# Optimization experiments

Measured on AMD Instinct MI355X. Metric: run time of the kernel, lower is better.

## Reference

```python
import jax, jax.numpy as jnp
import numpy as np

B, L, D, H, DK, DV = 512, 256, 1024, 16, 64, 64
TEMP = float(np.sqrt(D))  # source uses sqrt(d_model), not sqrt(d_k)
LN_EPS = 1.0              # LayerNormalization default eps=1, added to std


def setup_inputs() -> dict:
    key = jax.random.key(0)
    ks = jax.random.split(key, 7)
    u = lambda k, shape: jax.random.uniform(k, shape, jnp.float32, -0.04, 0.04)
    return {
        "q": jax.random.normal(ks[0], (B, D), jnp.float32),
        "k": jax.random.normal(ks[1], (B, L, D), jnp.float32),
        "v": jax.random.normal(ks[2], (B, L, D), jnp.float32),
        "Wq": u(ks[3], (H, DK, D)),   # stacked per-head q-proj weights
        "Wk": u(ks[4], (H, DK, D)),
        "Wv": u(ks[5], (H, DV, D)),
        "Wp": u(ks[6], (D, H * DV)),  # output projection (nn.Linear weight layout)
        "scale": jnp.ones((D,), jnp.float32),
        "offset": jnp.zeros((D,), jnp.float32),
    }


def reference(q, k, v, Wq, Wk, Wv, Wp, scale, offset):
    # per-head projections (batched over heads instead of a Python loop)
    hq = jnp.einsum('bd,hkd->bhk', q, Wq)       # [B,H,DK]
    hk = jnp.einsum('bld,hkd->bhlk', k, Wk)     # [B,H,L,DK]
    hv = jnp.einsum('bld,hvd->bhlv', v, Wv)     # [B,H,L,DV]
    # single-query dot-product attention per head
    scores = jnp.einsum('bhk,bhlk->bhl', hq, hk) / TEMP
    w = jax.nn.softmax(scores, axis=-1)         # dropout is identity (rate 0 / eval)
    ctx = jnp.einsum('bhl,bhlv->bhv', w, hv).reshape(B, H * DV)
    # output projection + residual
    out = ctx @ Wp.T + q
    # LayerNormalization: unbiased std (torch.std default), eps added to std
    mean = out.mean(axis=-1, keepdims=True)
    std = jnp.sqrt(jnp.sum((out - mean) ** 2, axis=-1, keepdims=True) / (D - 1))
    return scale * (out - mean) / (std + LN_EPS) + offset
```

## Files before the change

kernel.cpp:

```cpp
#include <hip/hip_runtime.h>

#define B_ 512
#define L_ 256
#define D_ 1024
#define H_ 16
#define DK_ 64
#define DV_ 64

typedef float f32x4 __attribute__((ext_vector_type(4)));
typedef __bf16 bf16x8 __attribute__((ext_vector_type(8)));

#define MFMA16(a, b, c) __builtin_amdgcn_mfma_f32_16x16x32_bf16((a), (b), (c), 0, 0, 0)

__device__ inline bf16x8 cvt8(f32x4 a, f32x4 b) {
  bf16x8 r;
  r[0] = (__bf16)a[0]; r[1] = (__bf16)a[1]; r[2] = (__bf16)a[2]; r[3] = (__bf16)a[3];
  r[4] = (__bf16)b[0]; r[5] = (__bf16)b[1]; r[6] = (__bf16)b[2]; r[7] = (__bf16)b[3];
  return r;
}

__global__ __launch_bounds__(256) void k_hq(const float* __restrict__ q,
                                            const float* __restrict__ Wq,
                                            __bf16* __restrict__ hq) {
  int tid = threadIdx.x, lane = tid & 63, wid = tid >> 6;
  int r16 = lane & 15, g = lane >> 4;
  int n0 = (blockIdx.x * 4 + wid) * 16;
  int m0 = blockIdx.y * 16;
  const float* arow = q  + (size_t)(m0 + r16) * D_;
  const float* brow = Wq + (size_t)(n0 + r16) * D_;
  f32x4 acc = {0.f, 0.f, 0.f, 0.f};
  for (int ks = 0; ks < D_ / 32; ++ks) {
    int k0 = ks * 32 + g * 8;
    f32x4 a0 = *(const f32x4*)(arow + k0);
    f32x4 a1 = *(const f32x4*)(arow + k0 + 4);
    f32x4 b0 = *(const f32x4*)(brow + k0);
    f32x4 b1 = *(const f32x4*)(brow + k0 + 4);
    acc = MFMA16(cvt8(a0, a1), cvt8(b0, b1), acc);
  }
#pragma unroll
  for (int r = 0; r < 4; ++r) {
    int m = m0 + g * 4 + r;
    hq[(size_t)m * (H_ * DK_) + n0 + r16] = (__bf16)acc[r];
  }
}

__global__ __launch_bounds__(256) void k_aq(const __bf16* __restrict__ hq,
                                            const float* __restrict__ Wk,
                                            __bf16* __restrict__ Aq) {
  int tid = threadIdx.x, lane = tid & 63, wid = tid >> 6;
  int r16 = lane & 15, g = lane >> 4;
  int h = blockIdx.z;
  int n0 = (blockIdx.x * 4 + wid) * 16;
  int m0 = blockIdx.y * 16;
  const __bf16* arow = hq + (size_t)(m0 + r16) * (H_ * DK_) + h * DK_;
  const float* bcol = Wk + (size_t)h * DK_ * D_ + n0 + r16;
  f32x4 acc = {0.f, 0.f, 0.f, 0.f};
#pragma unroll
  for (int ks = 0; ks < 2; ++ks) {
    int k0 = ks * 32 + g * 8;
    bf16x8 a = *(const bf16x8*)(arow + k0);
    f32x4 c0, c1;
#pragma unroll
    for (int j = 0; j < 4; ++j) c0[j] = bcol[(size_t)(k0 + j) * D_];
#pragma unroll
    for (int j = 0; j < 4; ++j) c1[j] = bcol[(size_t)(k0 + 4 + j) * D_];
    acc = MFMA16(a, cvt8(c0, c1), acc);
  }
#pragma unroll
  for (int r = 0; r < 4; ++r) {
    int m = m0 + g * 4 + r;
    Aq[(size_t)m * (H_ * D_) + (size_t)h * D_ + n0 + r16] = (__bf16)acc[r];
  }
}

__global__ __launch_bounds__(512) void k_attn(const float* __restrict__ kg,
                                              const float* __restrict__ vg,
                                              const __bf16* __restrict__ Aq,
                                              __bf16* __restrict__ cv) {
  __shared__ float  s_lds[H_][L_ + 4];
  __shared__ __bf16 w_lds[H_][L_ + 8];

  int b = blockIdx.x;
  int tid = threadIdx.x, lane = tid & 63, wv = tid >> 6;
  int r16 = lane & 15, g = lane >> 4;
  const __bf16* AqB = Aq + (size_t)b * H_ * D_;
  const float*  kB  = kg + (size_t)b * L_ * D_;
  const float*  vB  = vg + (size_t)b * L_ * D_;

  f32x4 accA[2] = {{0.f,0.f,0.f,0.f}, {0.f,0.f,0.f,0.f}};
  for (int ks = 0; ks < D_ / 32; ++ks) {
    int k0 = ks * 32 + g * 8;
    bf16x8 a = *(const bf16x8*)(AqB + (size_t)r16 * D_ + k0);
#pragma unroll
    for (int nt = 0; nt < 2; ++nt) {
      int l = wv * 32 + nt * 16 + r16;
      const float* p = kB + (size_t)l * D_ + k0;
      accA[nt] = MFMA16(a, cvt8(*(const f32x4*)p, *(const f32x4*)(p + 4)), accA[nt]);
    }
  }
  const float inv_temp = 1.0f / 32.0f;
#pragma unroll
  for (int nt = 0; nt < 2; ++nt)
#pragma unroll
    for (int r = 0; r < 4; ++r)
      s_lds[g * 4 + r][wv * 32 + nt * 16 + r16] = accA[nt][r] * inv_temp;
  __syncthreads();

#pragma unroll
  for (int rr = 0; rr < 2; ++rr) {
    int row = wv * 2 + rr;
    float x0 = s_lds[row][lane];
    float x1 = s_lds[row][lane + 64];
    float x2 = s_lds[row][lane + 128];
    float x3 = s_lds[row][lane + 192];
    float m = fmaxf(fmaxf(x0, x1), fmaxf(x2, x3));
#pragma unroll
    for (int off = 32; off; off >>= 1) m = fmaxf(m, __shfl_xor(m, off));
    float e0 = __expf(x0 - m), e1 = __expf(x1 - m);
    float e2 = __expf(x2 - m), e3 = __expf(x3 - m);
    float s = e0 + e1 + e2 + e3;
#pragma unroll
    for (int off = 32; off; off >>= 1) s += __shfl_xor(s, off);
    float inv = 1.0f / s;
    w_lds[row][lane]       = (__bf16)(e0 * inv);
    w_lds[row][lane + 64]  = (__bf16)(e1 * inv);
    w_lds[row][lane + 128] = (__bf16)(e2 * inv);
    w_lds[row][lane + 192] = (__bf16)(e3 * inv);
  }
  __syncthreads();

  bf16x8 afr[8];
#pragma unroll
  for (int ksl = 0; ksl < 8; ++ksl)
    afr[ksl] = *(const bf16x8*)(&w_lds[r16][ksl * 32 + g * 8]);

#pragma unroll
  for (int nt = 0; nt < 8; ++nt) {
    int d = wv * 128 + nt * 16 + r16;
    f32x4 c = {0.f, 0.f, 0.f, 0.f};
#pragma unroll
    for (int ksl = 0; ksl < 8; ++ksl) {
      int l0 = ksl * 32 + g * 8;
      const float* p = vB + (size_t)l0 * D_ + d;
      f32x4 c0, c1;
#pragma unroll
      for (int j = 0; j < 4; ++j) c0[j] = p[(size_t)j * D_];
#pragma unroll
      for (int j = 0; j < 4; ++j) c1[j] = p[(size_t)(4 + j) * D_];
      c = MFMA16(afr[ksl], cvt8(c0, c1), c);
    }
#pragma unroll
    for (int r = 0; r < 4; ++r)
      cv[(size_t)b * (H_ * D_) + (size_t)(g * 4 + r) * D_ + d] = (__bf16)c[r];
  }
}

__global__ __launch_bounds__(256) void k_ctx(const __bf16* __restrict__ cv,
                                             const float* __restrict__ Wv,
                                             __bf16* __restrict__ ctx) {
  int tid = threadIdx.x, lane = tid & 63, wid = tid >> 6;
  int r16 = lane & 15, g = lane >> 4;
  int h = blockIdx.z, m0 = blockIdx.y * 16, n0 = wid * 16;
  const __bf16* arow = cv + (size_t)(m0 + r16) * (H_ * D_) + (size_t)h * D_;
  const float* brow = Wv + (size_t)h * DV_ * D_ + (size_t)(n0 + r16) * D_;
  f32x4 acc = {0.f, 0.f, 0.f, 0.f};
  for (int ks = 0; ks < D_ / 32; ++ks) {
    int k0 = ks * 32 + g * 8;
    bf16x8 a = *(const bf16x8*)(arow + k0);
    f32x4 b0 = *(const f32x4*)(brow + k0);
    f32x4 b1 = *(const f32x4*)(brow + k0 + 4);
    acc = MFMA16(a, cvt8(b0, b1), acc);
  }
#pragma unroll
  for (int r = 0; r < 4; ++r) {
    int m = m0 + g * 4 + r;
    ctx[(size_t)m * (H_ * DV_) + h * DV_ + n0 + r16] = (__bf16)acc[r];
  }
}

__global__ __launch_bounds__(256) void k_out(const __bf16* __restrict__ ctx,
                                             const float* __restrict__ Wp,
                                             const float* __restrict__ q,
                                             float* __restrict__ outp) {
  int tid = threadIdx.x, lane = tid & 63, wid = tid >> 6;
  int r16 = lane & 15, g = lane >> 4;
  int n0 = (blockIdx.x * 4 + wid) * 16;
  int m0 = blockIdx.y * 16;
  const __bf16* arow = ctx + (size_t)(m0 + r16) * D_;
  const float* brow = Wp + (size_t)(n0 + r16) * D_;
  f32x4 acc = {0.f, 0.f, 0.f, 0.f};
  for (int ks = 0; ks < D_ / 32; ++ks) {
    int k0 = ks * 32 + g * 8;
    bf16x8 a = *(const bf16x8*)(arow + k0);
    f32x4 b0 = *(const f32x4*)(brow + k0);
    f32x4 b1 = *(const f32x4*)(brow + k0 + 4);
    acc = MFMA16(a, cvt8(b0, b1), acc);
  }
#pragma unroll
  for (int r = 0; r < 4; ++r) {
    int m = m0 + g * 4 + r;
    outp[(size_t)m * D_ + n0 + r16] = acc[r] + q[(size_t)m * D_ + n0 + r16];
  }
}

__global__ __launch_bounds__(256) void k_ln(const float* __restrict__ xin,
                                            const float* __restrict__ scale,
                                            const float* __restrict__ offs,
                                            float* __restrict__ out) {
  __shared__ float red[4];
  int b = blockIdx.x, tid = threadIdx.x;
  const float* row = xin + (size_t)b * D_;
  f32x4 x = *(const f32x4*)(row + tid * 4);
  float s = x[0] + x[1] + x[2] + x[3];
#pragma unroll
  for (int off = 32; off; off >>= 1) s += __shfl_xor(s, off);
  if ((tid & 63) == 0) red[tid >> 6] = s;
  __syncthreads();
  float mean = (red[0] + red[1] + red[2] + red[3]) * (1.0f / D_);
  __syncthreads();
  float vs = 0.f;
#pragma unroll
  for (int j = 0; j < 4; ++j) { float d = x[j] - mean; vs += d * d; }
#pragma unroll
  for (int off = 32; off; off >>= 1) vs += __shfl_xor(vs, off);
  if ((tid & 63) == 0) red[tid >> 6] = vs;
  __syncthreads();
  float var = (red[0] + red[1] + red[2] + red[3]) * (1.0f / (D_ - 1));
  float inv = 1.0f / (sqrtf(var) + 1.0f);
  f32x4 sc = *(const f32x4*)(scale + tid * 4);
  f32x4 of = *(const f32x4*)(offs + tid * 4);
  f32x4 o;
#pragma unroll
  for (int j = 0; j < 4; ++j) o[j] = sc[j] * (x[j] - mean) * inv + of[j];
  *(f32x4*)(out + (size_t)b * D_ + tid * 4) = o;
}

extern "C" void kernel_launch(void* const* d_in, const int* in_sizes, int n_in,
                              void* d_out, int out_size, void* d_ws, size_t ws_size,
                              hipStream_t stream) {
  const float* q     = (const float*)d_in[0];
  const float* k     = (const float*)d_in[1];
  const float* v     = (const float*)d_in[2];
  const float* Wq    = (const float*)d_in[3];
  const float* Wk    = (const float*)d_in[4];
  const float* Wv    = (const float*)d_in[5];
  const float* Wp    = (const float*)d_in[6];
  const float* scale = (const float*)d_in[7];
  const float* offs  = (const float*)d_in[8];
  float* out = (float*)d_out;

  char* ws = (char*)d_ws;
  __bf16* hq  = (__bf16*)(ws);
  __bf16* Aq  = (__bf16*)(ws + (size_t)1  * (1 << 20));
  __bf16* cv  = (__bf16*)(ws + (size_t)17 * (1 << 20));
  __bf16* ctx = (__bf16*)(ws + (size_t)33 * (1 << 20));
  float*  outp = (float*)(ws + (size_t)34 * (1 << 20));

  k_hq  <<<dim3(16, 32),      256, 0, stream>>>(q, Wq, hq);
  k_aq  <<<dim3(16, 32, 16),  256, 0, stream>>>(hq, Wk, Aq);
  k_attn<<<dim3(512),         512, 0, stream>>>(k, v, Aq, cv);
  k_ctx <<<dim3(1, 32, 16),   256, 0, stream>>>(cv, Wv, ctx);
  k_out <<<dim3(16, 32),      256, 0, stream>>>(ctx, Wp, q, outp);
  k_ln  <<<dim3(512),         256, 0, stream>>>(outp, scale, offs, out);
}
```

Before: 374.5 us.

## Split attention kernel into score and coalesced fp32 weighted-V kernels

The fused per-batch attention kernel is split into a score kernel (more blocks, one 16-row L tile per wave) that writes fp32 scores to workspace, and a weighted-sum kernel that recomputes softmax and accumulates weights times V with plain FMAs. The V read changes from strided scalar column loads feeding MFMA to coalesced float2 row loads, with the softmax weights broadcast from LDS. The goal is better memory coalescing and more parallelism on the bandwidth-bound K/V streams. The cost is an extra launch, a workspace round trip for the scores, and CUDA-core FMAs in place of matrix instructions for the V product.

```diff
diff --git a/kernel.cpp b/kernel.cpp
--- a/kernel.cpp
+++ b/kernel.cpp
@@ -8,7 +8,9 @@
 #define DV_ 64
 
 typedef float f32x4 __attribute__((ext_vector_type(4)));
+typedef float f32x2 __attribute__((ext_vector_type(2)));
 typedef __bf16 bf16x8 __attribute__((ext_vector_type(8)));
+typedef __bf16 bf16x2 __attribute__((ext_vector_type(2)));
 
 #define MFMA16(a, b, c) __builtin_amdgcn_mfma_f32_16x16x32_bf16((a), (b), (c), 0, 0, 0)
 
@@ -73,46 +75,47 @@
   }
 }
 
-__global__ __launch_bounds__(512) void k_attn(const float* __restrict__ kg,
-                                              const float* __restrict__ vg,
-                                              const __bf16* __restrict__ Aq,
-                                              __bf16* __restrict__ cv) {
-  __shared__ float  s_lds[H_][L_ + 4];
-  __shared__ __bf16 w_lds[H_][L_ + 8];
-
-  int b = blockIdx.x;
+__global__ __launch_bounds__(256) void k_score(const float* __restrict__ kg,
+                                               const __bf16* __restrict__ Aq,
+                                               float* __restrict__ sc) {
   int tid = threadIdx.x, lane = tid & 63, wv = tid >> 6;
   int r16 = lane & 15, g = lane >> 4;
+  int b = blockIdx.y;
+  int l0 = blockIdx.x * 64 + wv * 16;
   const __bf16* AqB = Aq + (size_t)b * H_ * D_;
-  const float*  kB  = kg + (size_t)b * L_ * D_;
-  const float*  vB  = vg + (size_t)b * L_ * D_;
-
-  f32x4 accA[2] = {{0.f,0.f,0.f,0.f}, {0.f,0.f,0.f,0.f}};
+  const float*  kR  = kg + ((size_t)b * L_ + l0 + r16) * D_;
+  f32x4 acc = {0.f, 0.f, 0.f, 0.f};
+#pragma unroll 4
   for (int ks = 0; ks < D_ / 32; ++ks) {
     int k0 = ks * 32 + g * 8;
     bf16x8 a = *(const bf16x8*)(AqB + (size_t)r16 * D_ + k0);
-#pragma unroll
-    for (int nt = 0; nt < 2; ++nt) {
-      int l = wv * 32 + nt * 16 + r16;
-      const float* p = kB + (size_t)l * D_ + k0;
-      accA[nt] = MFMA16(a, cvt8(*(const f32x4*)p, *(const f32x4*)(p + 4)), accA[nt]);
-    }
-  }
-  const float inv_temp = 1.0f / 32.0f;
-#pragma unroll
-  for (int nt = 0; nt < 2; ++nt)
-#pragma unroll
-    for (int r = 0; r < 4; ++r)
-      s_lds[g * 4 + r][wv * 32 + nt * 16 + r16] = accA[nt][r] * inv_temp;
-  __syncthreads();
-
-#pragma unroll
-  for (int rr = 0; rr < 2; ++rr) {
-    int row = wv * 2 + rr;
-    float x0 = s_lds[row][lane];
-    float x1 = s_lds[row][lane + 64];
-    float x2 = s_lds[row][lane + 128];
-    float x3 = s_lds[row][lane + 192];
+    f32x4 b0 = *(const f32x4*)(kR + k0);
+    f32x4 b1 = *(const f32x4*)(kR + k0 + 4);
+    acc = MFMA16(a, cvt8(b0, b1), acc);
+  }
+#pragma unroll
+  for (int r = 0; r < 4; ++r) {
+    int h = g * 4 + r;
+    sc[((size_t)b * H_ + h) * L_ + l0 + r16] = acc[r] * 0.03125f;
+  }
+}
+
+#define WPAD 20
+__global__ __launch_bounds__(256) void k_cv(const float* __restrict__ vg,
+                                            const float* __restrict__ sc,
+                                            __bf16* __restrict__ cv) {
+  __shared__ float wT[L_][WPAD];
+
+  int tid = threadIdx.x, lane = tid & 63, wv = tid >> 6;
+  int b = blockIdx.y;
+
+  const float* scB = sc + (size_t)b * H_ * L_;
+#pragma unroll
+  for (int rr = 0; rr < 4; ++rr) {
+    int row = wv * 4 + rr;
+    const float* srow = scB + (size_t)row * L_;
+    float x0 = srow[lane], x1 = srow[lane + 64];
+    float x2 = srow[lane + 128], x3 = srow[lane + 192];
     float m = fmaxf(fmaxf(x0, x1), fmaxf(x2, x3));
 #pragma unroll
     for (int off = 32; off; off >>= 1) m = fmaxf(m, __shfl_xor(m, off));
@@ -122,36 +125,40 @@
 #pragma unroll
     for (int off = 32; off; off >>= 1) s += __shfl_xor(s, off);
     float inv = 1.0f / s;
-    w_lds[row][lane]       = (__bf16)(e0 * inv);
-    w_lds[row][lane + 64]  = (__bf16)(e1 * inv);
-    w_lds[row][lane + 128] = (__bf16)(e2 * inv);
-    w_lds[row][lane + 192] = (__bf16)(e3 * inv);
-  }
-  __syncthreads();
-
-  bf16x8 afr[8];
-#pragma unroll
-  for (int ksl = 0; ksl < 8; ++ksl)
-    afr[ksl] = *(const bf16x8*)(&w_lds[r16][ksl * 32 + g * 8]);
-
-#pragma unroll
-  for (int nt = 0; nt < 8; ++nt) {
-    int d = wv * 128 + nt * 16 + r16;
-    f32x4 c = {0.f, 0.f, 0.f, 0.f};
-#pragma unroll
-    for (int ksl = 0; ksl < 8; ++ksl) {
-      int l0 = ksl * 32 + g * 8;
-      const float* p = vB + (size_t)l0 * D_ + d;
-      f32x4 c0, c1;
-#pragma unroll
-      for (int j = 0; j < 4; ++j) c0[j] = p[(size_t)j * D_];
-#pragma unroll
-      for (int j = 0; j < 4; ++j) c1[j] = p[(size_t)(4 + j) * D_];
-      c = MFMA16(afr[ksl], cvt8(c0, c1), c);
+    wT[lane]      [row] = e0 * inv;
+    wT[lane + 64] [row] = e1 * inv;
+    wT[lane + 128][row] = e2 * inv;
+    wT[lane + 192][row] = e3 * inv;
+  }
+  __syncthreads();
+
+  int c0 = blockIdx.x * 512 + tid * 2;
+  const float* vB = vg + (size_t)b * L_ * D_ + c0;
+  f32x2 acc[16];
+#pragma unroll
+  for (int h = 0; h < 16; ++h) acc[h] = (f32x2){0.f, 0.f};
+
+#pragma unroll 2
+  for (int l = 0; l < L_; ++l) {
+    f32x2 v2 = *(const f32x2*)(vB + (size_t)l * D_);
+    f32x4 w0 = *(const f32x4*)(&wT[l][0]);
+    f32x4 w1 = *(const f32x4*)(&wT[l][4]);
+    f32x4 w2 = *(const f32x4*)(&wT[l][8]);
+    f32x4 w3 = *(const f32x4*)(&wT[l][12]);
+#pragma unroll
+    for (int j = 0; j < 4; ++j) {
+      acc[j]      += w0[j] * v2;
+      acc[4 + j]  += w1[j] * v2;
+      acc[8 + j]  += w2[j] * v2;
+      acc[12 + j] += w3[j] * v2;
     }
-#pragma unroll
-    for (int r = 0; r < 4; ++r)
-      cv[(size_t)b * (H_ * D_) + (size_t)(g * 4 + r) * D_ + d] = (__bf16)c[r];
+  }
+#pragma unroll
+  for (int h = 0; h < 16; ++h) {
+    bf16x2 o;
+    o[0] = (__bf16)acc[h][0];
+    o[1] = (__bf16)acc[h][1];
+    *(bf16x2*)(cv + ((size_t)b * H_ + h) * D_ + c0) = o;
   }
 }
 
@@ -250,16 +257,18 @@
   float* out = (float*)d_out;
 
   char* ws = (char*)d_ws;
-  __bf16* hq  = (__bf16*)(ws);
-  __bf16* Aq  = (__bf16*)(ws + (size_t)1  * (1 << 20));
-  __bf16* cv  = (__bf16*)(ws + (size_t)17 * (1 << 20));
-  __bf16* ctx = (__bf16*)(ws + (size_t)33 * (1 << 20));
-  float*  outp = (float*)(ws + (size_t)34 * (1 << 20));
-
-  k_hq  <<<dim3(16, 32),      256, 0, stream>>>(q, Wq, hq);
-  k_aq  <<<dim3(16, 32, 16),  256, 0, stream>>>(hq, Wk, Aq);
-  k_attn<<<dim3(512),         512, 0, stream>>>(k, v, Aq, cv);
-  k_ctx <<<dim3(1, 32, 16),   256, 0, stream>>>(cv, Wv, ctx);
-  k_out <<<dim3(16, 32),      256, 0, stream>>>(ctx, Wp, q, outp);
-  k_ln  <<<dim3(512),         256, 0, stream>>>(outp, scale, offs, out);
-}
+  __bf16* hq   = (__bf16*)(ws);
+  __bf16* Aq   = (__bf16*)(ws + (size_t)1  * (1 << 20));
+  float*  scr  = (float*) (ws + (size_t)17 * (1 << 20));
+  __bf16* cv   = (__bf16*)(ws + (size_t)25 * (1 << 20));
+  __bf16* ctx  = (__bf16*)(ws + (size_t)41 * (1 << 20));
+  float*  outp = (float*) (ws + (size_t)42 * (1 << 20));
+
+  k_hq   <<<dim3(16, 32),     256, 0, stream>>>(q, Wq, hq);
+  k_aq   <<<dim3(16, 32, 16), 256, 0, stream>>>(hq, Wk, Aq);
+  k_score<<<dim3(4, 512),     256, 0, stream>>>(k, Aq, scr);
+  k_cv   <<<dim3(2, 512),     256, 0, stream>>>(v, scr, cv);
+  k_ctx  <<<dim3(1, 32, 16),  256, 0, stream>>>(cv, Wv, ctx);
+  k_out  <<<dim3(16, 32),     256, 0, stream>>>(ctx, Wp, q, outp);
+  k_ln   <<<dim3(512),        256, 0, stream>>>(outp, scale, offs, out);
+}
```

Result: faster. 317.6 us (-15.2%).
